# Kernel optimization log

Measured on AMD Instinct MI355X. Metric: run time of the kernel, lower is better.

## Reference

```python
import jax, jax.numpy as jnp
import numpy as np

N, P, S, CORE, H, HEADS, B = 49152, 256, 256, 192, 256, 8, 1
D = H // HEADS  # head_dim = 32
EPS = 1e-5


def setup_inputs() -> dict:
    key = jax.random.key(0)
    ks = jax.random.split(key, 8)
    x = jax.random.normal(ks[0], (B, N, H), dtype=jnp.float32)
    # cores tile all N nodes exactly once (KMeans-like partition), plus random overlap ring
    core = jnp.arange(N, dtype=jnp.int32).reshape(P, CORE)
    ov = jax.random.randint(ks[1], (P, S - CORE), 0, N, dtype=jnp.int32)
    patch_idx = jnp.concatenate([core, ov], axis=1)                      # [P,S]
    core_mask = jnp.concatenate(
        [jnp.ones((P, CORE), bool), jnp.zeros((P, S - CORE), bool)], axis=1)  # [P,S]
    def w(k):
        return jax.random.normal(k, (H, H), dtype=jnp.float32) * 0.02
    return dict(
        x=x, patch_idx=patch_idx, core_mask=core_mask,
        Wq=w(ks[2]), bq=jnp.zeros((H,), jnp.float32),
        Wk=w(ks[3]), bk=jnp.zeros((H,), jnp.float32),
        Wv=w(ks[4]), bv=jnp.zeros((H,), jnp.float32),
        Wo=w(ks[5]), bo=jnp.zeros((H,), jnp.float32),
        ln_g=jnp.ones((H,), jnp.float32), ln_b=jnp.zeros((H,), jnp.float32),
    )


def reference(x, patch_idx, core_mask, Wq, bq, Wk, bk, Wv, bv, Wo, bo, ln_g, ln_b):
    # x: [B,N,H]; patch_idx: [P,S] int; core_mask: [P,S] bool
    px = x[:, patch_idx]                                   # gather -> [B,P,S,H]
    def proj(W, b):
        return (px @ W.T + b).reshape(B, P, S, HEADS, D)
    Q, K, V = proj(Wq, bq), proj(Wk, bk), proj(Wv, bv)
    scores = jnp.einsum('bpihd,bpjhd->bphij', Q, K) / jnp.sqrt(jnp.float32(D))
    attn = jax.nn.softmax(scores, axis=-1)                 # dropout is identity in eval
    att = jnp.einsum('bphij,bpjhd->bpihd', attn, V).reshape(B, P, S, H)
    out = att @ Wo.T + bo                                  # [B,P,S,H]
    # scatter-add only core slots back to nodes, track update counts
    contrib = jnp.where(core_mask[None, :, :, None], out, 0.0).reshape(B, P * S, H)
    flat = patch_idx.reshape(-1)
    acc = jnp.zeros((B, N, H), x.dtype).at[:, flat].add(contrib)
    cnt = jnp.zeros((N,), x.dtype).at[flat].add(core_mask.reshape(-1).astype(x.dtype))
    acc = acc / jnp.clip(cnt, 1.0)[None, :, None]
    # residual + LayerNorm (biased variance, as torch)
    y = x + acc
    mu = jnp.mean(y, axis=-1, keepdims=True)
    var = jnp.var(y, axis=-1, keepdims=True)
    return (y - mu) / jnp.sqrt(var + EPS) * ln_g + ln_b
```

## Files before the change

kernel.cpp:

```cpp
#include <hip/hip_runtime.h>

#define PP 256
#define SS 256
#define CORE_ 192
#define HH 256
#define NHEAD 8
#define DD 32

typedef __attribute__((ext_vector_type(4))) float f32x4;
typedef __attribute__((ext_vector_type(8))) short s8v;
typedef __attribute__((ext_vector_type(4))) short s4v;

__device__ __forceinline__ float bf2f(unsigned short u) {
    union { unsigned int i; float f; } c; c.i = ((unsigned int)u) << 16; return c.f;
}
__device__ __forceinline__ unsigned short f2bf(float f) {
    union { float f; unsigned int i; } c; c.f = f;
    unsigned int i = c.i;
    return (unsigned short)((i + 0x7fffu + ((i >> 16) & 1u)) >> 16);
}

__device__ __forceinline__ void gload16(const unsigned short* g, unsigned short* l) {
    __builtin_amdgcn_global_load_lds(
        (const __attribute__((address_space(1))) void*)g,
        (__attribute__((address_space(3))) void*)l, 16, 0, 0);
}

#define SW(row, chunk) ((chunk) ^ (((row) >> 1) & 3))

__global__ __launch_bounds__(256) void k_prep(
    const float* __restrict__ Wq, const float* __restrict__ Wk,
    const float* __restrict__ Wv, const float* __restrict__ Wo,
    const float* __restrict__ bq, const float* __restrict__ bk,
    const float* __restrict__ bv,
    unsigned short* __restrict__ Wb, float* __restrict__ bb) {
    int bid = blockIdx.x, tid = threadIdx.x;
    if (bid >= 256) {
        int which = bid - 256;
        const float* b = which == 0 ? bq : which == 1 ? bk : bv;
        bb[which * 256 + tid] = b[tid];
        return;
    }
    int i = bid * 256 + tid;
    int row = i >> 6;
    int col4 = (i & 63) * 4;
    const float* src = row < 256 ? Wq : row < 512 ? Wk : row < 768 ? Wv : Wo;
    float4 v = *(const float4*)(src + (size_t)(row & 255) * 256 + col4);
    s4v w;
    w[0] = (short)f2bf(v.x); w[1] = (short)f2bf(v.y);
    w[2] = (short)f2bf(v.z); w[3] = (short)f2bf(v.w);
    *(s4v*)(Wb + (size_t)row * 256 + col4) = w;
}

__global__ __launch_bounds__(256) void k_qkv(
    const float* __restrict__ x, const int* __restrict__ pidx,
    const unsigned short* __restrict__ Wb, const float* __restrict__ bb,
    unsigned short* __restrict__ qkv) {
    int p = blockIdx.x, mt = blockIdx.y, ng = blockIdx.z;
    if (ng == 0 && mt == 3) return;
    __shared__ unsigned short As[64][32];
    __shared__ unsigned short Bs[256][32];
    int tid = threadIdx.x;
    int wave = tid >> 6, lane = tid & 63;
    int g = lane >> 4, c0 = lane & 15;
    f32x4 acc[4][4] = {};
    int arow = tid >> 2, aseg = tid & 3;
    int node = pidx[p * SS + mt * 64 + arow];
    const float* asrc = x + (size_t)node * HH + aseg * 8;
    const unsigned short* wsrc = Wb + (size_t)ng * 256 * 256;

    for (int k0 = 0; k0 < HH; k0 += 32) {
#pragma unroll
        for (int j = 0; j < 4; ++j) {
            int chunk = j * 256 + wave * 64 + lane;
            int row = chunk >> 2, c8 = chunk & 3;
            gload16(wsrc + (size_t)row * 256 + k0 + c8 * 8,
                    &Bs[0][0] + (size_t)(j * 256 + wave * 64) * 8);
        }
        float4 v0 = *(const float4*)(asrc + k0);
        float4 v1 = *(const float4*)(asrc + k0 + 4);
        s8v aw;
        aw[0] = (short)f2bf(v0.x); aw[1] = (short)f2bf(v0.y);
        aw[2] = (short)f2bf(v0.z); aw[3] = (short)f2bf(v0.w);
        aw[4] = (short)f2bf(v1.x); aw[5] = (short)f2bf(v1.y);
        aw[6] = (short)f2bf(v1.z); aw[7] = (short)f2bf(v1.w);
        *(s8v*)&As[arow][SW(arow, aseg) * 8] = aw;
        __syncthreads();
        s8v af[4], bfv[4];
#pragma unroll
        for (int m2 = 0; m2 < 4; ++m2) {
            int r = m2 * 16 + c0;
            af[m2] = *(const s8v*)&As[r][SW(r, g) * 8];
        }
#pragma unroll
        for (int nt = 0; nt < 4; ++nt) {
            int r = wave * 64 + nt * 16 + c0;
            bfv[nt] = *(const s8v*)&Bs[r][g * 8];
        }
#pragma unroll
        for (int m2 = 0; m2 < 4; ++m2)
#pragma unroll
            for (int nt = 0; nt < 4; ++nt)
                acc[m2][nt] = __builtin_amdgcn_mfma_f32_16x16x32_bf16(
                    af[m2], bfv[nt], acc[m2][nt], 0, 0, 0);
        __syncthreads();
    }
#pragma unroll
    for (int nt = 0; nt < 4; ++nt) {
        int ncol = wave * 64 + nt * 16 + c0;
        float bv_ = bb[ng * 256 + ncol];
#pragma unroll
        for (int m2 = 0; m2 < 4; ++m2)
#pragma unroll
            for (int r = 0; r < 4; ++r) {
                int srow = mt * 64 + m2 * 16 + g * 4 + r;
                qkv[((size_t)p * SS + srow) * 768 + ng * 256 + ncol] =
                    f2bf(acc[m2][nt][r] + bv_);
            }
    }
}

__global__ __launch_bounds__(256) void k_attn(
    const unsigned short* __restrict__ qkv, unsigned short* __restrict__ att) {
    int p = blockIdx.x, h = blockIdx.y;
    __shared__ unsigned short Ks[256][32];
    __shared__ unsigned short Vt[32][256];
    __shared__ unsigned short Pb[4][16][256];
    int tid = threadIdx.x;
    int wave = tid >> 6, lane = tid & 63;
    int g = lane >> 4, c0 = lane & 15;

#pragma unroll
    for (int j = 0; j < 4; ++j) {
        int chunk = j * 256 + wave * 64 + lane;
        int row = chunk >> 2, c8 = chunk & 3;
        gload16(qkv + ((size_t)p * SS + row) * 768 + 256 + h * DD + c8 * 8,
                &Ks[0][0] + (size_t)(j * 256 + wave * 64) * 8);
    }
    {
        int chunk = tid & 3, rb = tid >> 2;
#pragma unroll
        for (int pass = 0; pass < 4; ++pass) {
            int row = rb + pass * 64;
            s8v vv = *(const s8v*)(qkv + ((size_t)p * SS + row) * 768 + 512 + h * DD + chunk * 8);
            int cj = row >> 3, jo = row & 7;
#pragma unroll
            for (int e = 0; e < 8; ++e) {
                int d = chunk * 8 + e;
                Vt[d][((cj ^ ((d >> 1) & 7)) << 3) + jo] = (unsigned short)vv[e];
            }
        }
    }
    __syncthreads();

    const float scale = 0.17677669529663687f;
    int cs = (c0 >> 1) & 7;

    for (int mi = 0; mi < 3; ++mi) {
        int q0 = (wave * 3 + mi) * 16;
        s8v qa = *(const s8v*)(qkv + ((size_t)p * SS + q0 + c0) * 768 + h * DD + g * 8);
        f32x4 sacc[16];
#pragma unroll
        for (int jt = 0; jt < 16; ++jt) {
            int row = jt * 16 + c0;
            s8v kf = *(const s8v*)&Ks[row][g * 8];
            sacc[jt] = __builtin_amdgcn_mfma_f32_16x16x32_bf16(
                qa, kf, f32x4{0.f, 0.f, 0.f, 0.f}, 0, 0, 0);
        }
        float linv[4];
#pragma unroll
        for (int r = 0; r < 4; ++r) {
            float mx = sacc[0][r];
#pragma unroll
            for (int jt = 1; jt < 16; ++jt) mx = fmaxf(mx, sacc[jt][r]);
#pragma unroll
            for (int off = 1; off < 16; off <<= 1)
                mx = fmaxf(mx, __shfl_xor(mx, off, 64));
            float sum = 0.f;
#pragma unroll
            for (int jt = 0; jt < 16; ++jt) {
                float e = __expf((sacc[jt][r] - mx) * scale);
                sacc[jt][r] = e;
                sum += e;
            }
#pragma unroll
            for (int off = 1; off < 16; off <<= 1)
                sum += __shfl_xor(sum, off, 64);
            linv[r] = 1.f / sum;
            int qq = g * 4 + r;
            int qs = (qq >> 1) & 7;
            unsigned short* prow = &Pb[wave][qq][0];
#pragma unroll
            for (int jt = 0; jt < 16; ++jt) {
                int j0 = jt * 2 + (c0 >> 3);
                prow[((j0 ^ qs) << 3) + (c0 & 7)] = (unsigned short)f2bf(sacc[jt][r]);
            }
        }
        asm volatile("s_waitcnt lgkmcnt(0)" ::: "memory");
        __builtin_amdgcn_sched_barrier(0);
        f32x4 oacc[2] = {f32x4{0.f, 0.f, 0.f, 0.f}, f32x4{0.f, 0.f, 0.f, 0.f}};
#pragma unroll
        for (int kt = 0; kt < 8; ++kt) {
            s8v pa = *(const s8v*)&Pb[wave][c0][(((kt * 4 + g) ^ cs) << 3)];
#pragma unroll
            for (int nt = 0; nt < 2; ++nt) {
                int d = nt * 16 + c0;
                s8v vb = *(const s8v*)&Vt[d][(((kt * 4 + g) ^ ((d >> 1) & 7)) << 3)];
                oacc[nt] = __builtin_amdgcn_mfma_f32_16x16x32_bf16(
                    pa, vb, oacc[nt], 0, 0, 0);
            }
        }
        asm volatile("s_waitcnt lgkmcnt(0)" ::: "memory");
        __builtin_amdgcn_sched_barrier(0);
#pragma unroll
        for (int nt = 0; nt < 2; ++nt)
#pragma unroll
            for (int r = 0; r < 4; ++r) {
                int qq = g * 4 + r;
                att[((size_t)p * CORE_ + q0 + qq) * HH + h * DD + nt * 16 + c0] =
                    f2bf(oacc[nt][r] * linv[r]);
            }
    }
}

__global__ __launch_bounds__(256) void k_out(
    const unsigned short* __restrict__ att, const float* __restrict__ x,
    const unsigned short* __restrict__ Wb, const float* __restrict__ bo,
    const float* __restrict__ ln_g, const float* __restrict__ ln_b,
    float* __restrict__ out) {
    int p = blockIdx.x, mb = blockIdx.y;
    __shared__ unsigned short As[64][32];
    __shared__ unsigned short Bs[256][32];
    int tid = threadIdx.x;
    int wave = tid >> 6, lane = tid & 63;
    int g = lane >> 4, c0 = lane & 15;
    f32x4 acc[16] = {};

    for (int k0 = 0; k0 < HH; k0 += 32) {
        {
            int chunk = wave * 64 + lane;
            int row = chunk >> 2, c8 = chunk & 3;
            gload16(att + ((size_t)p * CORE_ + mb * 64 + row) * HH + k0 + c8 * 8,
                    &As[0][0] + (size_t)(wave * 64) * 8);
        }
#pragma unroll
        for (int j = 0; j < 4; ++j) {
            int chunk = j * 256 + wave * 64 + lane;
            int row = chunk >> 2, c8 = chunk & 3;
            gload16(Wb + (size_t)(768 + row) * 256 + k0 + c8 * 8,
                    &Bs[0][0] + (size_t)(j * 256 + wave * 64) * 8);
        }
        __syncthreads();
        int ar = wave * 16 + c0;
        s8v af = *(const s8v*)&As[ar][g * 8];
#pragma unroll
        for (int nt = 0; nt < 16; ++nt) {
            int r = nt * 16 + c0;
            s8v bfv = *(const s8v*)&Bs[r][g * 8];
            acc[nt] = __builtin_amdgcn_mfma_f32_16x16x32_bf16(af, bfv, acc[nt], 0, 0, 0);
        }
        __syncthreads();
    }
    int srow0 = mb * 64 + wave * 16 + g * 4;
    float sum[4] = {0, 0, 0, 0}, ssq[4] = {0, 0, 0, 0};
#pragma unroll
    for (int nt = 0; nt < 16; ++nt) {
        int col = nt * 16 + c0;
        float bov = bo[col];
#pragma unroll
        for (int r = 0; r < 4; ++r) {
            size_t node = (size_t)p * CORE_ + srow0 + r;
            float v = acc[nt][r] + bov + x[node * HH + col];
            acc[nt][r] = v;
            sum[r] += v; ssq[r] += v * v;
        }
    }
#pragma unroll
    for (int off = 1; off < 16; off <<= 1) {
#pragma unroll
        for (int r = 0; r < 4; ++r) {
            sum[r] += __shfl_xor(sum[r], off, 64);
            ssq[r] += __shfl_xor(ssq[r], off, 64);
        }
    }
#pragma unroll
    for (int r = 0; r < 4; ++r) {
        float mu = sum[r] * (1.f / HH);
        float var = ssq[r] * (1.f / HH) - mu * mu;
        float rstd = rsqrtf(var + 1e-5f);
        size_t node = (size_t)p * CORE_ + srow0 + r;
#pragma unroll
        for (int nt = 0; nt < 16; ++nt) {
            int col = nt * 16 + c0;
            out[node * HH + col] = (acc[nt][r] - mu) * rstd * ln_g[col] + ln_b[col];
        }
    }
}

extern "C" void kernel_launch(void* const* d_in, const int* in_sizes, int n_in,
                              void* d_out, int out_size, void* d_ws, size_t ws_size,
                              hipStream_t stream) {
    const float* x   = (const float*)d_in[0];
    const int* pidx  = (const int*)d_in[1];
    const float* Wq  = (const float*)d_in[3];
    const float* bq  = (const float*)d_in[4];
    const float* Wk  = (const float*)d_in[5];
    const float* bk  = (const float*)d_in[6];
    const float* Wv  = (const float*)d_in[7];
    const float* bv  = (const float*)d_in[8];
    const float* Wo  = (const float*)d_in[9];
    const float* bo  = (const float*)d_in[10];
    const float* lng = (const float*)d_in[11];
    const float* lnb = (const float*)d_in[12];

    unsigned short* qkv = (unsigned short*)d_ws;
    unsigned short* att = qkv + (size_t)PP * SS * 768;
    unsigned short* Wb  = att + (size_t)PP * CORE_ * HH;
    float* bb = (float*)(Wb + 1024 * 256);

    k_prep<<<259, 256, 0, stream>>>(Wq, Wk, Wv, Wo, bq, bk, bv, Wb, bb);
    k_qkv<<<dim3(PP, 4, 3), 256, 0, stream>>>(x, pidx, Wb, bb, qkv);
    k_attn<<<dim3(PP, NHEAD), 256, 0, stream>>>(qkv, att);
    k_out<<<dim3(PP, 3), 256, 0, stream>>>(att, x, Wb, bo, lng, lnb, (float*)d_out);
}
```

Before: 166.9 us.

## Pre-swizzle weight and intermediate layouts in global memory and double-buffer GEMM tiles

Weights converted in k_prep are written with an XOR-swizzled column layout, and the K part of qkv and the att output use the same swizzle. LDS tiles filled by direct global-to-LDS loads therefore come out bank-conflict-free without extra address math. The qkv and out GEMMs also double-buffer their LDS tiles so the next K slice loads while MFMAs run on the current one. This costs twice the LDS and a more complex layout contract between kernels, which must stay consistent in every reader.

```diff
diff --git a/kernel.cpp b/kernel.cpp
--- a/kernel.cpp
+++ b/kernel.cpp
@@ -27,6 +27,9 @@
 }
 
 #define SW(row, chunk) ((chunk) ^ (((row) >> 1) & 3))
+__device__ __forceinline__ int swcol(int c, int row) {
+    return (c & ~31) | (((((c >> 3) & 3) ^ ((row >> 1) & 3))) << 3) | (c & 7);
+}
 
 __global__ __launch_bounds__(256) void k_prep(
     const float* __restrict__ Wq, const float* __restrict__ Wk,
@@ -35,21 +38,26 @@
     const float* __restrict__ bv,
     unsigned short* __restrict__ Wb, float* __restrict__ bb) {
     int bid = blockIdx.x, tid = threadIdx.x;
-    if (bid >= 256) {
-        int which = bid - 256;
+    if (bid >= 128) {
+        int which = bid - 128;
         const float* b = which == 0 ? bq : which == 1 ? bk : bv;
         bb[which * 256 + tid] = b[tid];
         return;
     }
-    int i = bid * 256 + tid;
-    int row = i >> 6;
-    int col4 = (i & 63) * 4;
+    int c = bid * 256 + tid;
+    int row = c >> 5;
+    int within = c & 31;
+    int w = within >> 2, sl = within & 3;
     const float* src = row < 256 ? Wq : row < 512 ? Wk : row < 768 ? Wv : Wo;
-    float4 v = *(const float4*)(src + (size_t)(row & 255) * 256 + col4);
-    s4v w;
-    w[0] = (short)f2bf(v.x); w[1] = (short)f2bf(v.y);
-    w[2] = (short)f2bf(v.z); w[3] = (short)f2bf(v.w);
-    *(s4v*)(Wb + (size_t)row * 256 + col4) = w;
+    const float* sp = src + (size_t)(row & 255) * 256 + w * 32 + SW(row, sl) * 8;
+    float4 a = *(const float4*)sp;
+    float4 b4 = *(const float4*)(sp + 4);
+    s8v wv;
+    wv[0] = (short)f2bf(a.x); wv[1] = (short)f2bf(a.y);
+    wv[2] = (short)f2bf(a.z); wv[3] = (short)f2bf(a.w);
+    wv[4] = (short)f2bf(b4.x); wv[5] = (short)f2bf(b4.y);
+    wv[6] = (short)f2bf(b4.z); wv[7] = (short)f2bf(b4.w);
+    *(s8v*)(Wb + (size_t)row * 256 + w * 32 + sl * 8) = wv;
 }
 
 __global__ __launch_bounds__(256) void k_qkv(
@@ -58,8 +66,8 @@
     unsigned short* __restrict__ qkv) {
     int p = blockIdx.x, mt = blockIdx.y, ng = blockIdx.z;
     if (ng == 0 && mt == 3) return;
-    __shared__ unsigned short As[64][32];
-    __shared__ unsigned short Bs[256][32];
+    __shared__ unsigned short As[2][64][32];
+    __shared__ unsigned short Bs[2][256][32];
     int tid = threadIdx.x;
     int wave = tid >> 6, lane = tid & 63;
     int g = lane >> 4, c0 = lane & 15;
@@ -69,13 +77,13 @@
     const float* asrc = x + (size_t)node * HH + aseg * 8;
     const unsigned short* wsrc = Wb + (size_t)ng * 256 * 256;
 
-    for (int k0 = 0; k0 < HH; k0 += 32) {
+    auto stage = [&](int k0, int b) {
 #pragma unroll
         for (int j = 0; j < 4; ++j) {
             int chunk = j * 256 + wave * 64 + lane;
             int row = chunk >> 2, c8 = chunk & 3;
             gload16(wsrc + (size_t)row * 256 + k0 + c8 * 8,
-                    &Bs[0][0] + (size_t)(j * 256 + wave * 64) * 8);
+                    &Bs[b][0][0] + (size_t)(j * 256 + wave * 64) * 8);
         }
         float4 v0 = *(const float4*)(asrc + k0);
         float4 v1 = *(const float4*)(asrc + k0 + 4);
@@ -84,18 +92,25 @@
         aw[2] = (short)f2bf(v0.z); aw[3] = (short)f2bf(v0.w);
         aw[4] = (short)f2bf(v1.x); aw[5] = (short)f2bf(v1.y);
         aw[6] = (short)f2bf(v1.z); aw[7] = (short)f2bf(v1.w);
-        *(s8v*)&As[arow][SW(arow, aseg) * 8] = aw;
-        __syncthreads();
+        *(s8v*)&As[b][arow][SW(arow, aseg) * 8] = aw;
+    };
+
+    stage(0, 0);
+    __syncthreads();
+#pragma unroll
+    for (int ks = 0; ks < 8; ++ks) {
+        int b = ks & 1;
+        if (ks < 7) stage((ks + 1) * 32, b ^ 1);
         s8v af[4], bfv[4];
 #pragma unroll
         for (int m2 = 0; m2 < 4; ++m2) {
             int r = m2 * 16 + c0;
-            af[m2] = *(const s8v*)&As[r][SW(r, g) * 8];
+            af[m2] = *(const s8v*)&As[b][r][SW(r, g) * 8];
         }
 #pragma unroll
         for (int nt = 0; nt < 4; ++nt) {
             int r = wave * 64 + nt * 16 + c0;
-            bfv[nt] = *(const s8v*)&Bs[r][g * 8];
+            bfv[nt] = *(const s8v*)&Bs[b][r][SW(r, g) * 8];
         }
 #pragma unroll
         for (int m2 = 0; m2 < 4; ++m2)
@@ -114,7 +129,8 @@
 #pragma unroll
             for (int r = 0; r < 4; ++r) {
                 int srow = mt * 64 + m2 * 16 + g * 4 + r;
-                qkv[((size_t)p * SS + srow) * 768 + ng * 256 + ncol] =
+                int sc = (ng == 1) ? swcol(ncol, srow) : ncol;
+                qkv[((size_t)p * SS + srow) * 768 + ng * 256 + sc] =
                     f2bf(acc[m2][nt][r] + bv_);
             }
     }
@@ -163,7 +179,7 @@
 #pragma unroll
         for (int jt = 0; jt < 16; ++jt) {
             int row = jt * 16 + c0;
-            s8v kf = *(const s8v*)&Ks[row][g * 8];
+            s8v kf = *(const s8v*)&Ks[row][SW(row, g) * 8];
             sacc[jt] = __builtin_amdgcn_mfma_f32_16x16x32_bf16(
                 qa, kf, f32x4{0.f, 0.f, 0.f, 0.f}, 0, 0, 0);
         }
@@ -217,7 +233,9 @@
 #pragma unroll
             for (int r = 0; r < 4; ++r) {
                 int qq = g * 4 + r;
-                att[((size_t)p * CORE_ + q0 + qq) * HH + h * DD + nt * 16 + c0] =
+                int crow = q0 + qq;
+                int c = h * DD + nt * 16 + c0;
+                att[((size_t)p * CORE_ + crow) * HH + swcol(c, crow)] =
                     f2bf(oacc[nt][r] * linv[r]);
             }
     }
@@ -229,34 +247,41 @@
     const float* __restrict__ ln_g, const float* __restrict__ ln_b,
     float* __restrict__ out) {
     int p = blockIdx.x, mb = blockIdx.y;
-    __shared__ unsigned short As[64][32];
-    __shared__ unsigned short Bs[256][32];
+    __shared__ unsigned short As[2][64][32];
+    __shared__ unsigned short Bs[2][256][32];
     int tid = threadIdx.x;
     int wave = tid >> 6, lane = tid & 63;
     int g = lane >> 4, c0 = lane & 15;
     f32x4 acc[16] = {};
 
-    for (int k0 = 0; k0 < HH; k0 += 32) {
+    auto stage = [&](int k0, int b) {
         {
             int chunk = wave * 64 + lane;
             int row = chunk >> 2, c8 = chunk & 3;
             gload16(att + ((size_t)p * CORE_ + mb * 64 + row) * HH + k0 + c8 * 8,
-                    &As[0][0] + (size_t)(wave * 64) * 8);
+                    &As[b][0][0] + (size_t)(wave * 64) * 8);
         }
 #pragma unroll
         for (int j = 0; j < 4; ++j) {
             int chunk = j * 256 + wave * 64 + lane;
             int row = chunk >> 2, c8 = chunk & 3;
             gload16(Wb + (size_t)(768 + row) * 256 + k0 + c8 * 8,
-                    &Bs[0][0] + (size_t)(j * 256 + wave * 64) * 8);
-        }
-        __syncthreads();
+                    &Bs[b][0][0] + (size_t)(j * 256 + wave * 64) * 8);
+        }
+    };
+
+    stage(0, 0);
+    __syncthreads();
+#pragma unroll
+    for (int ks = 0; ks < 8; ++ks) {
+        int b = ks & 1;
+        if (ks < 7) stage((ks + 1) * 32, b ^ 1);
         int ar = wave * 16 + c0;
-        s8v af = *(const s8v*)&As[ar][g * 8];
+        s8v af = *(const s8v*)&As[b][ar][SW(ar, g) * 8];
 #pragma unroll
         for (int nt = 0; nt < 16; ++nt) {
             int r = nt * 16 + c0;
-            s8v bfv = *(const s8v*)&Bs[r][g * 8];
+            s8v bfv = *(const s8v*)&Bs[b][r][SW(r, g) * 8];
             acc[nt] = __builtin_amdgcn_mfma_f32_16x16x32_bf16(af, bfv, acc[nt], 0, 0, 0);
         }
         __syncthreads();
@@ -318,7 +343,7 @@
     unsigned short* Wb  = att + (size_t)PP * CORE_ * HH;
     float* bb = (float*)(Wb + 1024 * 256);
 
-    k_prep<<<259, 256, 0, stream>>>(Wq, Wk, Wv, Wo, bq, bk, bv, Wb, bb);
+    k_prep<<<131, 256, 0, stream>>>(Wq, Wk, Wv, Wo, bq, bk, bv, Wb, bb);
     k_qkv<<<dim3(PP, 4, 3), 256, 0, stream>>>(x, pidx, Wb, bb, qkv);
     k_attn<<<dim3(PP, NHEAD), 256, 0, stream>>>(qkv, att);
     k_out<<<dim3(PP, 3), 256, 0, stream>>>(att, x, Wb, bo, lng, lnb, (float*)d_out);
```

Measured after the change: 159.3 us. 4.5% less time.
